# Kernel optimization log

Measured on AMD Instinct MI355X. Metric: run time of the kernel, lower is better.

## Reference

```python
import jax, jax.numpy as jnp
import numpy as np

NUM_CODES = 100000
DIM = 64
N = 65536   # B*T flattened visits
L = 48      # max codes per visit (padded with -1)
C = 1.0     # Poincare ball curvature
MIN_NORM = 1e-15
BALL_EPS = 1e-5   # geoopt projx boundary eps for float32
ATANH_EPS = 1e-7  # clamp artanh argument below 1


def _projx(x):
    # Poincare ball projection: pull points with norm >= (1-eps)/sqrt(c) back inside.
    sqrt_c = jnp.sqrt(C)
    norm = jnp.maximum(jnp.linalg.norm(x, axis=-1, keepdims=True), MIN_NORM)
    maxnorm = (1.0 - BALL_EPS) / sqrt_c
    return jnp.where(norm > maxnorm, x * (maxnorm / norm), x)


def setup_inputs() -> dict:
    key = jax.random.key(0)
    k1, k2, k3 = jax.random.split(key, 3)
    emb = jax.random.normal(k1, (NUM_CODES, DIM), dtype=jnp.float32) * 0.001
    emb = _projx(emb)
    ids = jax.random.randint(k2, (N, L), 0, NUM_CODES)
    pad = jax.random.uniform(k3, (N, L)) < 0.3
    code_ids = jnp.where(pad, jnp.int64(-1) if jax.config.jax_enable_x64 else -1, ids)
    return {"code_ids": code_ids, "emb": emb}


def reference(code_ids, emb):
    # code_ids: [N, L] int, -1 = padding; emb: [NUM_CODES, DIM] Poincare points.
    sqrt_c = jnp.sqrt(jnp.asarray(C, emb.dtype))
    mask = code_ids >= 0                               # [N, L]
    safe_ids = jnp.where(mask, code_ids, 0)
    x = emb[safe_ids]                                  # [N, L, D] gather
    # logmap0: artanh(sqrt(c)*||x||) * x / (sqrt(c)*||x||)
    norm = jnp.maximum(jnp.linalg.norm(x, axis=-1, keepdims=True), MIN_NORM)
    arg = jnp.minimum(sqrt_c * norm, 1.0 - ATANH_EPS)
    tangents = (jnp.arctanh(arg) / (sqrt_c * norm)) * x  # [N, L, D]
    m = mask[..., None].astype(emb.dtype)
    s = jnp.sum(tangents * m, axis=1)                  # [N, D]
    cnt = jnp.sum(m, axis=1)                           # [N, 1]
    return s / jnp.maximum(cnt, 1.0)                   # zeros for empty visits
```

## Files before the change

kernel.cpp:

```cpp
#include <hip/hip_runtime.h>


#define LCODES 48
#define DIM 64

typedef float vf4 __attribute__((ext_vector_type(4)));

__global__ __launch_bounds__(256)
void amax_kernel(const float* __restrict__ emb, unsigned* __restrict__ bmax,
                 long n4) {
    const uint4* __restrict__ u4 = reinterpret_cast<const uint4*>(emb);
    const long T = (long)gridDim.x * 256;
    unsigned m = 0;
    for (long i = (long)blockIdx.x * 256 + threadIdx.x; i < n4; i += 2 * T) {
        const uint4 a = u4[i];
        m = max(m, a.x & 0x7fffffffu);
        m = max(m, a.y & 0x7fffffffu);
        m = max(m, a.z & 0x7fffffffu);
        m = max(m, a.w & 0x7fffffffu);
        if (i + T < n4) {
            const uint4 b = u4[i + T];
            m = max(m, b.x & 0x7fffffffu);
            m = max(m, b.y & 0x7fffffffu);
            m = max(m, b.z & 0x7fffffffu);
            m = max(m, b.w & 0x7fffffffu);
        }
    }
    #pragma unroll
    for (int d = 1; d <= 32; d <<= 1)
        m = max(m, (unsigned)__shfl_xor((int)m, d, 64));
    __shared__ unsigned sm[4];
    if ((threadIdx.x & 63) == 0) sm[threadIdx.x >> 6] = m;
    __syncthreads();
    if (threadIdx.x == 0)
        bmax[blockIdx.x] = max(max(sm[0], sm[1]), max(sm[2], sm[3]));
}

__device__ __forceinline__ float global_amax1024(const unsigned* __restrict__ bmax) {
    const int lane = threadIdx.x & 63;
    unsigned m = 0;
    #pragma unroll
    for (int k = 0; k < 16; ++k)
        m = max(m, bmax[lane + 64 * k]);
    #pragma unroll
    for (int d = 1; d <= 32; d <<= 1)
        m = max(m, (unsigned)__shfl_xor((int)m, d, 64));
    return __uint_as_float(m);
}

__global__ __launch_bounds__(256)
void build_i8_kernel(const float* __restrict__ emb,
                     const unsigned* __restrict__ bmax,
                     unsigned char* __restrict__ tab,
                     float* __restrict__ qsout, int C) {
    const float amax = global_amax1024(bmax);
    const float qs   = amax * (1.0006f / 127.f);
    const float invq = (amax > 0.f) ? (127.f / (amax * 1.0006f)) : 0.f;
    if (blockIdx.x == 0 && threadIdx.x == 0) qsout[0] = qs;
    if (blockIdx.x == 0 && threadIdx.x < 16)
        reinterpret_cast<unsigned*>(tab + (size_t)C * DIM)[threadIdx.x] = 0u;

    const int tid  = threadIdx.x;
    const int lane = tid & 63;
    const int wave = tid >> 6;
    const int g = lane >> 3, s = lane & 7;
    const int r = blockIdx.x * 32 + wave * 8 + g;
    if (r >= C) return;

    const float4* __restrict__ emb4 = reinterpret_cast<const float4*>(emb);
    const float4 a = emb4[r * 16 + 2 * s];
    const float4 b = emb4[r * 16 + 2 * s + 1];

    float ss = a.x*a.x + a.y*a.y + a.z*a.z + a.w*a.w
             + b.x*b.x + b.y*b.y + b.z*b.z + b.w*b.w;
    ss += __shfl_xor(ss, 1, 64);
    ss += __shfl_xor(ss, 2, 64);
    ss += __shfl_xor(ss, 4, 64);

    float scale;
    if (__builtin_expect(ss > 0.04f, 0)) {
        const float norm = fmaxf(sqrtf(ss), 1e-15f);
        const float arg  = fminf(norm, 1.f - 1e-7f);
        scale = 0.5f * logf((1.f + arg) / (1.f - arg)) / norm;
    } else {
        scale = 1.f + ss * (0.33333333333f + ss * (0.2f + ss * 0.14285714285f));
    }
    scale *= invq;

    const float t[8] = { a.x*scale, a.y*scale, a.z*scale, a.w*scale,
                         b.x*scale, b.y*scale, b.z*scale, b.w*scale };
    unsigned u[8];
    #pragma unroll
    for (int k = 0; k < 8; ++k)
        u[k] = (unsigned)((int)rintf(t[k]) + 128);

    uint2 w;
    w.x = u[0] | (u[1] << 8) | (u[2] << 16) | (u[3] << 24);
    w.y = u[4] | (u[5] << 8) | (u[6] << 16) | (u[7] << 24);
    reinterpret_cast<uint2*>(tab)[r * 8 + s] = w;
}

__global__ __launch_bounds__(256)
void visit_gather_i8q_kernel(const int* __restrict__ ids,
                             const unsigned char* __restrict__ tab,
                             const float* __restrict__ qsp,
                             float* __restrict__ out, int N, int C) {
    const float qs = qsp[0];

    const int tid  = threadIdx.x;
    const int lane = tid & 63;
    const int wave = tid >> 6;
    const int v0   = (blockIdx.x * 4 + wave) * 4;
    if (v0 >= N) return;

    __shared__ int sids[4][4 * LCODES];

    int m0 = -1, m1 = -1, m2 = -1, m3 = -1;
    if (lane < LCODES) {
        const long b = (long)v0 * LCODES;
        m0 = __builtin_nontemporal_load(&ids[b + lane]);
        if (v0 + 1 < N) m1 = __builtin_nontemporal_load(&ids[b + LCODES + lane]);
        if (v0 + 2 < N) m2 = __builtin_nontemporal_load(&ids[b + 2 * LCODES + lane]);
        if (v0 + 3 < N) m3 = __builtin_nontemporal_load(&ids[b + 3 * LCODES + lane]);
        sids[wave][lane]              = m0;
        sids[wave][LCODES + lane]     = m1;
        sids[wave][2 * LCODES + lane] = m2;
        sids[wave][3 * LCODES + lane] = m3;
    }
    const float cnt0 = (float)__popcll(__ballot(m0 >= 0));
    const float cnt1 = (float)__popcll(__ballot(m1 >= 0));
    const float cnt2 = (float)__popcll(__ballot(m2 >= 0));
    const float cnt3 = (float)__popcll(__ballot(m3 >= 0));

    const int v = lane >> 4;
    const int g = (lane >> 2) & 3;
    const int s = lane & 3;
    const uint4* __restrict__ tab4 = reinterpret_cast<const uint4*>(tab);
    const int* __restrict__ slid = &sids[wave][v * LCODES + g];

    unsigned aE[4] = {0,0,0,0}, aO[4] = {0,0,0,0};

    #pragma unroll
    for (int it = 0; it < LCODES / 4; ++it) {
        const int id = slid[4 * it];
        const unsigned base = ((unsigned)(id >= 0 ? id : C)) << 2;
        const uint4 w = tab4[base + s];
        aE[0] +=  w.x       & 0x00ff00ffu;
        aO[0] += (w.x >> 8) & 0x00ff00ffu;
        aE[1] +=  w.y       & 0x00ff00ffu;
        aO[1] += (w.y >> 8) & 0x00ff00ffu;
        aE[2] +=  w.z       & 0x00ff00ffu;
        aO[2] += (w.z >> 8) & 0x00ff00ffu;
        aE[3] +=  w.w       & 0x00ff00ffu;
        aO[3] += (w.w >> 8) & 0x00ff00ffu;
    }

    #pragma unroll
    for (int d = 4; d <= 8; d <<= 1) {
        #pragma unroll
        for (int k = 0; k < 4; ++k) {
            aE[k] += (unsigned)__shfl_xor((int)aE[k], d, 64);
            aO[k] += (unsigned)__shfl_xor((int)aO[k], d, 64);
        }
    }

    const int f   = lane & 15;
    const int src = (lane & 0x30) | (f >> 2);
    const int kk  = lane & 3;
    unsigned e = 0, o = 0;
    #pragma unroll
    for (int k = 0; k < 4; ++k) {
        const unsigned ek = (unsigned)__shfl((int)aE[k], src, 64);
        const unsigned ok = (unsigned)__shfl((int)aO[k], src, 64);
        if (kk == k) { e = ek; o = ok; }
    }
    const float cnt = (v == 0) ? cnt0 : (v == 1) ? cnt1 : (v == 2) ? cnt2 : cnt3;
    const float qinv  = qs / fmaxf(cnt, 1.f);
    const float fbias = 128.f * cnt;
    vf4 r;
    r.x = ((float)(e  & 0xffffu) - fbias) * qinv;
    r.y = ((float)(o  & 0xffffu) - fbias) * qinv;
    r.z = ((float)(e  >> 16)     - fbias) * qinv;
    r.w = ((float)(o  >> 16)     - fbias) * qinv;
    if (v0 + v < N) {
        vf4* o4 = reinterpret_cast<vf4*>(out);
        __builtin_nontemporal_store(r, &o4[(long)v0 * 16 + lane]);
    }
}

__global__ __launch_bounds__(256, 4)
void visit_fp32_kernel(const int* __restrict__ ids,
                       const float* __restrict__ emb,
                       float* __restrict__ out, int N) {
    const int tid  = threadIdx.x;
    const int lane = tid & 63;
    const int wave = tid >> 6;
    const int v    = blockIdx.x * 4 + wave;
    if (v >= N) return;

    int myid = -1;
    if (lane < LCODES) myid = ids[(long)v * LCODES + lane];
    const unsigned long long valid = __ballot(myid >= 0);
    const float cnt = (float)__popcll(valid);
    const int g = lane >> 3, s = lane & 7;
    const float4* __restrict__ emb4 = reinterpret_cast<const float4*>(emb);
    float4 accA = make_float4(0.f,0.f,0.f,0.f), accB = make_float4(0.f,0.f,0.f,0.f);
    #pragma unroll
    for (int it = 0; it < LCODES / 8; ++it) {
        const int id = __shfl(myid, it * 8 + g, 64);
        const float keep = (id >= 0) ? 1.f : 0.f;
        const unsigned base = ((unsigned)(id >= 0 ? id : 0)) << 4;
        float4 a = emb4[base + s], b = emb4[base + 8 + s];
        float ss = a.x*a.x + a.y*a.y + a.z*a.z + a.w*a.w
                 + b.x*b.x + b.y*b.y + b.z*b.z + b.w*b.w;
        ss += __shfl_xor(ss, 1, 64);
        ss += __shfl_xor(ss, 2, 64);
        ss += __shfl_xor(ss, 4, 64);
        float scale;
        if (__builtin_expect(__any(ss > 0.04f), 0)) {
            const float norm = fmaxf(sqrtf(ss), 1e-15f);
            const float arg  = fminf(norm, 1.f - 1e-7f);
            scale = 0.5f * logf((1.f + arg) / (1.f - arg)) / norm;
        } else {
            scale = 1.f + ss * (0.33333333333f + ss * (0.2f + ss * 0.14285714285f));
        }
        scale *= keep;
        accA.x += a.x*scale; accA.y += a.y*scale; accA.z += a.z*scale; accA.w += a.w*scale;
        accB.x += b.x*scale; accB.y += b.y*scale; accB.z += b.z*scale; accB.w += b.w*scale;
    }
    #pragma unroll
    for (int d = 8; d <= 32; d <<= 1) {
        accA.x += __shfl_xor(accA.x, d, 64); accA.y += __shfl_xor(accA.y, d, 64);
        accA.z += __shfl_xor(accA.z, d, 64); accA.w += __shfl_xor(accA.w, d, 64);
        accB.x += __shfl_xor(accB.x, d, 64); accB.y += __shfl_xor(accB.y, d, 64);
        accB.z += __shfl_xor(accB.z, d, 64); accB.w += __shfl_xor(accB.w, d, 64);
    }
    if (lane < 8) {
        const float inv = 1.f / fmaxf(cnt, 1.f);
        float4* o = reinterpret_cast<float4*>(out) + (long)v * (DIM / 4);
        o[2*s]   = make_float4(accA.x*inv, accA.y*inv, accA.z*inv, accA.w*inv);
        o[2*s+1] = make_float4(accB.x*inv, accB.y*inv, accB.z*inv, accB.w*inv);
    }
}

extern "C" void kernel_launch(void* const* d_in, const int* in_sizes, int n_in,
                              void* d_out, int out_size, void* d_ws, size_t ws_size,
                              hipStream_t stream) {
    const int*   ids = (const int*)d_in[0];
    const float* emb = (const float*)d_in[1];
    float*       out = (float*)d_out;

    const int N = in_sizes[0] / LCODES;
    const int C = in_sizes[1] / DIM;

    const size_t tab_off = 8192;
    const size_t need = tab_off + (size_t)(C + 1) * DIM;

    if (ws_size >= need) {
        unsigned*      bmax = (unsigned*)d_ws;
        float*         qsp  = (float*)((char*)d_ws + 4096);
        unsigned char* tab  = (unsigned char*)d_ws + tab_off;

        const long n4 = (long)C * DIM / 4;
        hipLaunchKernelGGL(amax_kernel, dim3(1024), dim3(256), 0, stream,
                           emb, bmax, n4);
        const int blocksA = (C + 31) / 32;
        hipLaunchKernelGGL(build_i8_kernel, dim3(blocksA), dim3(256), 0, stream,
                           emb, bmax, tab, qsp, C);
        const int blocksB = (N + 15) / 16;
        hipLaunchKernelGGL(visit_gather_i8q_kernel, dim3(blocksB), dim3(256), 0,
                           stream, ids, tab, qsp, out, N, C);
    } else {
        const int blocks = (N + 3) / 4;
        hipLaunchKernelGGL(visit_fp32_kernel, dim3(blocks), dim3(256), 0, stream,
                           ids, emb, out, N);
    }
}
```

Measured before the change: 106.4 us.

## Split int8 table into two dimension halves and gather per half in separate blocks

Result: slower. 113.7 us (+6.9%).

```diff
diff --git a/kernel.cpp b/kernel.cpp
--- a/kernel.cpp
+++ b/kernel.cpp
@@ -49,16 +49,18 @@
 }
 
 __global__ __launch_bounds__(256)
-void build_i8_kernel(const float* __restrict__ emb,
-                     const unsigned* __restrict__ bmax,
-                     unsigned char* __restrict__ tab,
-                     float* __restrict__ qsout, int C) {
+void build_i8h_kernel(const float* __restrict__ emb,
+                      const unsigned* __restrict__ bmax,
+                      unsigned char* __restrict__ tab,
+                      float* __restrict__ qsout, int C) {
     const float amax = global_amax1024(bmax);
     const float qs   = amax * (1.0006f / 127.f);
     const float invq = (amax > 0.f) ? (127.f / (amax * 1.0006f)) : 0.f;
     if (blockIdx.x == 0 && threadIdx.x == 0) qsout[0] = qs;
-    if (blockIdx.x == 0 && threadIdx.x < 16)
-        reinterpret_cast<unsigned*>(tab + (size_t)C * DIM)[threadIdx.x] = 0u;
+    if (blockIdx.x == 0 && threadIdx.x < 16) {
+        const int h = threadIdx.x >> 3, wd = threadIdx.x & 7;
+        reinterpret_cast<unsigned*>(tab)[((size_t)h * (C + 1) + C) * 8 + wd] = 0u;
+    }
 
     const int tid  = threadIdx.x;
     const int lane = tid & 63;
@@ -97,54 +99,62 @@
     uint2 w;
     w.x = u[0] | (u[1] << 8) | (u[2] << 16) | (u[3] << 24);
     w.y = u[4] | (u[5] << 8) | (u[6] << 16) | (u[7] << 24);
-    reinterpret_cast<uint2*>(tab)[r * 8 + s] = w;
+    const int h = s >> 2;
+    reinterpret_cast<uint2*>(tab)[((size_t)h * (C + 1) + r) * 4 + (s & 3)] = w;
 }
 
 __global__ __launch_bounds__(256)
-void visit_gather_i8q_kernel(const int* __restrict__ ids,
+void visit_gather_i8h_kernel(const int* __restrict__ ids,
                              const unsigned char* __restrict__ tab,
                              const float* __restrict__ qsp,
-                             float* __restrict__ out, int N, int C) {
+                             float* __restrict__ out, int N, int C, int bph) {
     const float qs = qsp[0];
 
     const int tid  = threadIdx.x;
     const int lane = tid & 63;
     const int wave = tid >> 6;
-    const int v0   = (blockIdx.x * 4 + wave) * 4;
+    const int bid  = blockIdx.x;
+    const int half = (bid >> 2) & 1;
+    const int vgrp = (bid >> 3) * 4 + (bid & 3);
+    if (vgrp >= bph) return;
+    const int v0 = vgrp * 32 + wave * 8;
     if (v0 >= N) return;
 
-    __shared__ int sids[4][4 * LCODES];
-
-    int m0 = -1, m1 = -1, m2 = -1, m3 = -1;
+    __shared__ int   sids[4][8 * 50];
+    __shared__ float scnt[4][8];
+
+    int m[8];
+    #pragma unroll
+    for (int r = 0; r < 8; ++r) m[r] = -1;
     if (lane < LCODES) {
-        const long b = (long)v0 * LCODES;
-        m0 = __builtin_nontemporal_load(&ids[b + lane]);
-        if (v0 + 1 < N) m1 = __builtin_nontemporal_load(&ids[b + LCODES + lane]);
-        if (v0 + 2 < N) m2 = __builtin_nontemporal_load(&ids[b + 2 * LCODES + lane]);
-        if (v0 + 3 < N) m3 = __builtin_nontemporal_load(&ids[b + 3 * LCODES + lane]);
-        sids[wave][lane]              = m0;
-        sids[wave][LCODES + lane]     = m1;
-        sids[wave][2 * LCODES + lane] = m2;
-        sids[wave][3 * LCODES + lane] = m3;
-    }
-    const float cnt0 = (float)__popcll(__ballot(m0 >= 0));
-    const float cnt1 = (float)__popcll(__ballot(m1 >= 0));
-    const float cnt2 = (float)__popcll(__ballot(m2 >= 0));
-    const float cnt3 = (float)__popcll(__ballot(m3 >= 0));
-
-    const int v = lane >> 4;
-    const int g = (lane >> 2) & 3;
-    const int s = lane & 3;
+        const long b = (long)v0 * LCODES + lane;
+        #pragma unroll
+        for (int r = 0; r < 8; ++r)
+            if (v0 + r < N)
+                m[r] = __builtin_nontemporal_load(&ids[b + (long)r * LCODES]);
+        #pragma unroll
+        for (int r = 0; r < 8; ++r) sids[wave][r * 50 + lane] = m[r];
+    }
+    #pragma unroll
+    for (int r = 0; r < 8; ++r) {
+        const float c = (float)__popcll(__ballot(m[r] >= 0));
+        if (lane == 0) scnt[wave][r] = c;
+    }
+
+    const int v = lane >> 3;
+    const int g = (lane >> 1) & 3;
+    const int s = lane & 1;
     const uint4* __restrict__ tab4 = reinterpret_cast<const uint4*>(tab);
-    const int* __restrict__ slid = &sids[wave][v * LCODES + g];
+    const unsigned hbase = (unsigned)(half * (C + 1) * 2 + s);
+    const int* __restrict__ slid = &sids[wave][v * 50 + g];
 
     unsigned aE[4] = {0,0,0,0}, aO[4] = {0,0,0,0};
 
     #pragma unroll
     for (int it = 0; it < LCODES / 4; ++it) {
         const int id = slid[4 * it];
-        const unsigned base = ((unsigned)(id >= 0 ? id : C)) << 2;
-        const uint4 w = tab4[base + s];
+        const unsigned row = (unsigned)(id >= 0 ? id : C);
+        const uint4 w = tab4[hbase + (row << 1)];
         aE[0] +=  w.x       & 0x00ff00ffu;
         aO[0] += (w.x >> 8) & 0x00ff00ffu;
         aE[1] +=  w.y       & 0x00ff00ffu;
@@ -156,7 +166,7 @@
     }
 
     #pragma unroll
-    for (int d = 4; d <= 8; d <<= 1) {
+    for (int d = 2; d <= 4; d <<= 1) {
         #pragma unroll
         for (int k = 0; k < 4; ++k) {
             aE[k] += (unsigned)__shfl_xor((int)aE[k], d, 64);
@@ -164,9 +174,9 @@
         }
     }
 
-    const int f   = lane & 15;
-    const int src = (lane & 0x30) | (f >> 2);
-    const int kk  = lane & 3;
+    const int f   = lane & 7;
+    const int src = (lane & 0x38) | (f >> 2);
+    const int kk  = f & 3;
     unsigned e = 0, o = 0;
     #pragma unroll
     for (int k = 0; k < 4; ++k) {
@@ -174,17 +184,18 @@
         const unsigned ok = (unsigned)__shfl((int)aO[k], src, 64);
         if (kk == k) { e = ek; o = ok; }
     }
-    const float cnt = (v == 0) ? cnt0 : (v == 1) ? cnt1 : (v == 2) ? cnt2 : cnt3;
+    const float cnt   = scnt[wave][lane >> 3];
     const float qinv  = qs / fmaxf(cnt, 1.f);
     const float fbias = 128.f * cnt;
     vf4 r;
-    r.x = ((float)(e  & 0xffffu) - fbias) * qinv;
-    r.y = ((float)(o  & 0xffffu) - fbias) * qinv;
-    r.z = ((float)(e  >> 16)     - fbias) * qinv;
-    r.w = ((float)(o  >> 16)     - fbias) * qinv;
-    if (v0 + v < N) {
+    r.x = ((float)(e & 0xffffu) - fbias) * qinv;
+    r.y = ((float)(o & 0xffffu) - fbias) * qinv;
+    r.z = ((float)(e >> 16)     - fbias) * qinv;
+    r.w = ((float)(o >> 16)     - fbias) * qinv;
+    const int vw = v0 + (lane >> 3);
+    if (vw < N) {
         vf4* o4 = reinterpret_cast<vf4*>(out);
-        __builtin_nontemporal_store(r, &o4[(long)v0 * 16 + lane]);
+        __builtin_nontemporal_store(r, &o4[(long)vw * 16 + half * 8 + f]);
     }
 }
 
@@ -265,11 +276,12 @@
         hipLaunchKernelGGL(amax_kernel, dim3(1024), dim3(256), 0, stream,
                            emb, bmax, n4);
         const int blocksA = (C + 31) / 32;
-        hipLaunchKernelGGL(build_i8_kernel, dim3(blocksA), dim3(256), 0, stream,
+        hipLaunchKernelGGL(build_i8h_kernel, dim3(blocksA), dim3(256), 0, stream,
                            emb, bmax, tab, qsp, C);
-        const int blocksB = (N + 15) / 16;
-        hipLaunchKernelGGL(visit_gather_i8q_kernel, dim3(blocksB), dim3(256), 0,
-                           stream, ids, tab, qsp, out, N, C);
+        const int bph = (N + 31) / 32;
+        const int blocksB = 8 * ((bph + 3) / 4);
+        hipLaunchKernelGGL(visit_gather_i8h_kernel, dim3(blocksB), dim3(256), 0,
+                           stream, ids, tab, qsp, out, N, C, bph);
     } else {
         const int blocks = (N + 3) / 4;
         hipLaunchKernelGGL(visit_fp32_kernel, dim3(blocks), dim3(256), 0, stream,
```
